# Performance work log

Measured on AMD Instinct MI355X. Metric: run time of the kernel, lower is better.

## Reference

```python
import jax, jax.numpy as jnp
import numpy as np

COUNT_BINS = 8
BOUND = 3.0
MIN_BIN_WIDTH = 1e-3
MIN_BIN_HEIGHT = 1e-3
MIN_DERIVATIVE = 1e-3
EPS = 1e-6


def _made_masks(D, H1, H2, M):
    indeg = np.arange(1, D + 1)                     # input degrees 1..D
    h1 = np.arange(H1) % (D - 1) + 1                # hidden degrees in [1, D-1]
    h2 = np.arange(H2) % (D - 1) + 1
    outdeg = np.tile(indeg, M)                      # (M*D,), reshape-compatible with (M, D)
    m1 = (h1[:, None] >= indeg[None, :]).astype(np.float32)   # (H1, D)
    m2 = (h2[:, None] >= h1[None, :]).astype(np.float32)      # (H2, H1)
    m3 = (outdeg[:, None] > h2[None, :]).astype(np.float32)   # (M*D, H2)
    return jnp.asarray(m1), jnp.asarray(m2), jnp.asarray(m3)


def _rq_spline_forward(x, w, h, d):
    # x: (B, D); w, h: (B, D, K) simplex weights; d: (B, D, K-1) softplus'd interior derivatives
    K = w.shape[-1]
    left, right = -BOUND, BOUND

    widths = MIN_BIN_WIDTH + (1.0 - MIN_BIN_WIDTH * K) * w
    heights = MIN_BIN_HEIGHT + (1.0 - MIN_BIN_HEIGHT * K) * h
    derivs = MIN_DERIVATIVE + d
    ones = jnp.ones_like(derivs[..., :1])
    derivs = jnp.concatenate([ones, derivs, ones], -1)          # (B, D, K+1), boundary slope 1

    cw = jnp.cumsum(widths, -1)
    edge_l = jnp.full_like(cw[..., :1], left)
    edge_r = jnp.full_like(cw[..., :1], right)
    cumw = jnp.concatenate([edge_l, left + (right - left) * cw[..., :-1], edge_r], -1)  # (B, D, K+1)
    widths = cumw[..., 1:] - cumw[..., :-1]
    ch = jnp.cumsum(heights, -1)
    cumh = jnp.concatenate([edge_l, left + (right - left) * ch[..., :-1], edge_r], -1)
    heights = cumh[..., 1:] - cumh[..., :-1]

    inside = (x >= left) & (x <= right)
    xc = jnp.clip(x, left, right)
    # pyro: bin_idx = sum(x >= cumwidths + eps) - 1
    idx = jnp.sum((xc[..., None] >= (cumw + EPS)).astype(jnp.int32), -1) - 1
    idx = jnp.clip(idx, 0, K - 1)                               # (B, D)

    def g(t):
        return jnp.take_along_axis(t, idx[..., None], axis=-1)[..., 0]

    x_k, w_k = g(cumw), g(widths)
    y_k, h_k = g(cumh), g(heights)
    delta = h_k / w_k
    d_k, d_k1 = g(derivs), g(derivs[..., 1:])

    theta = (xc - x_k) / w_k
    tt = theta * (1.0 - theta)
    num = h_k * (delta * theta ** 2 + d_k * tt)
    den = delta + (d_k + d_k1 - 2.0 * delta) * tt
    y = y_k + num / den
    dnum = delta ** 2 * (d_k1 * theta ** 2 + 2.0 * delta * tt + d_k * (1.0 - theta) ** 2)
    ld = jnp.log(dnum) - 2.0 * jnp.log(den)
    return jnp.where(inside, y, x), jnp.where(inside, ld, jnp.zeros_like(ld))


def _forward(x, W1, b1, W2, b2, W3, b3):
    B, D = x.shape
    H1, H2 = W1.shape[0], W2.shape[0]
    K = COUNT_BINS
    M = 3 * K - 1
    m1, m2, m3 = _made_masks(D, H1, H2, M)
    h1 = jax.nn.relu(x @ (W1 * m1).T + b1)
    h2 = jax.nn.relu(h1 @ (W2 * m2).T + b2)
    p = (h2 @ (W3 * m3).T + b3).reshape(B, M, D)                # (B, 3K-1, D)
    w = jax.nn.softmax(jnp.swapaxes(p[:, :K, :], 1, 2), axis=-1)          # (B, D, K)
    hgt = jax.nn.softmax(jnp.swapaxes(p[:, K:2 * K, :], 1, 2), axis=-1)   # (B, D, K)
    d = jax.nn.softplus(jnp.swapaxes(p[:, 2 * K:, :], 1, 2))              # (B, D, K-1)
    z, ld = _rq_spline_forward(x, w, hgt, d)
    return z, ld.sum(-1)


def setup_inputs() -> dict:
    key = jax.random.key(0)
    ks = jax.random.split(key, 7)
    B, D, H1, H2 = 32768, 64, 64, 32
    M = 3 * COUNT_BINS - 1
    s1, s2, s3 = 1.0 / np.sqrt(D), 1.0 / np.sqrt(H1), 1.0 / np.sqrt(H2)
    return {
        "x": jax.random.normal(ks[0], (B, D), jnp.float32),
        "W1": jax.random.uniform(ks[1], (H1, D), jnp.float32, -s1, s1),
        "b1": jax.random.uniform(ks[2], (H1,), jnp.float32, -s1, s1),
        "W2": jax.random.uniform(ks[3], (H2, H1), jnp.float32, -s2, s2),
        "b2": jax.random.uniform(ks[4], (H2,), jnp.float32, -s2, s2),
        "W3": jax.random.uniform(ks[5], (M * D, H2), jnp.float32, -s3, s3),
        "b3": jax.random.uniform(ks[6], (M * D,), jnp.float32, -s3, s3),
    }


def reference(x, W1, b1, W2, b2, W3, b3):
    return _forward(x, W1, b1, W2, b2, W3, b3)
```

## Files before the change

### kernel.cpp

```cpp
#include <hip/hip_runtime.h>

#define NM 23

typedef short short8 __attribute__((ext_vector_type(8)));
typedef float f32x4 __attribute__((ext_vector_type(4)));

__device__ __forceinline__ float softplus_f(float v) {
  return fmaxf(v, 0.f) + __logf(1.f + __expf(-fabsf(v)));
}

__device__ __forceinline__ float fastrcp(float v) {
  return __builtin_amdgcn_rcpf(v);
}

__device__ __forceinline__ unsigned short bf16_rne(float x) {
  unsigned u = __float_as_uint(x);
  u += 0x7FFFu + ((u >> 16) & 1u);
  return (unsigned short)(u >> 16);
}

__global__ __launch_bounds__(256) void prep_kernel(
    const float* __restrict__ W1, const float* __restrict__ W2,
    const float* __restrict__ W3,
    unsigned short* __restrict__ B1hi, unsigned short* __restrict__ B1lo,
    unsigned short* __restrict__ B2hi, unsigned short* __restrict__ B2lo,
    unsigned short* __restrict__ B3hi, unsigned short* __restrict__ B3lo) {
  const int idx = blockIdx.x * 256 + threadIdx.x;
  const int j = idx & 7, lane = (idx >> 3) & 63;
  const int col = lane & 15, quad = lane >> 4;

  if (idx < 4096) {
    const int rest = idx >> 9, kt = rest & 1, nt = rest >> 1;
    const int k = kt * 32 + quad * 8 + j;
    const int n = nt * 16 + col;
    const float v = ((n % 63) >= k) ? W1[n * 64 + k] : 0.f;
    const unsigned short h = bf16_rne(v);
    B1hi[idx] = h;
    B1lo[idx] = bf16_rne(v - __uint_as_float(((unsigned)h) << 16));
  }
  if (idx < 2048) {
    const int rest = idx >> 9, kt = rest & 1, nt = rest >> 1;
    const int k = kt * 32 + quad * 8 + j;
    const int n = nt * 16 + col;
    const float v = ((k % 63) <= n) ? W2[n * 64 + k] : 0.f;
    const unsigned short h = bf16_rne(v);
    B2hi[idx] = h;
    B2lo[idx] = bf16_rne(v - __uint_as_float(((unsigned)h) << 16));
  }
  if (idx < 92 * 64 * 8) {
    const int nt = idx >> 9;
    const int n = nt * 16 + col;
    const int d = n & 63;
    const int k = quad * 8 + j;
    const float v = (k < d) ? W3[(size_t)n * 32 + k] : 0.f;
    const unsigned short h = bf16_rne(v);
    B3hi[idx] = h;
    B3lo[idx] = bf16_rne(v - __uint_as_float(((unsigned)h) << 16));
  }
}

__device__ __forceinline__ void cvt_hilo(const float* src, short8& hi,
                                         short8& lo) {
  const f32x4 a0 = *reinterpret_cast<const f32x4*>(src);
  const f32x4 a1 = *reinterpret_cast<const f32x4*>(src + 4);
  const float af[8] = {a0.x, a0.y, a0.z, a0.w, a1.x, a1.y, a1.z, a1.w};
  #pragma unroll
  for (int j = 0; j < 8; ++j) {
    const unsigned short h = bf16_rne(af[j]);
    hi[j] = (short)h;
    lo[j] = (short)bf16_rne(af[j] - __uint_as_float(((unsigned)h) << 16));
  }
}

__global__ __launch_bounds__(256, 4) void fused_kernel(
    const float* __restrict__ x,
    const unsigned short* __restrict__ B1hi,
    const unsigned short* __restrict__ B1lo,
    const float* __restrict__ b1,
    const unsigned short* __restrict__ B2hi,
    const unsigned short* __restrict__ B2lo,
    const float* __restrict__ b2,
    const unsigned short* __restrict__ B3hi,
    const unsigned short* __restrict__ B3lo,
    const float* __restrict__ b3,
    float* __restrict__ out, int B) {
  __shared__ float h1s[64][68];
  __shared__ float h2s[64][36];
  __shared__ float b3s[64 * NM];

  const int t = threadIdx.x;
  const int b0 = blockIdx.x * 64;

  for (int idx = t; idx < 64 * NM; idx += 256) {
    const int dl = idx / NM, m = idx - dl * NM;
    b3s[idx] = b3[m * 64 + dl];
  }
  __syncthreads();

  const int lane = t & 63;
  const int wv   = __builtin_amdgcn_readfirstlane(t >> 6);
  const int mt   = wv;
  const int col  = lane & 15;
  const int quad = lane >> 4;
  const int arow = mt * 16 + col;

  {
    const float* xrow = x + (size_t)(b0 + arow) * 64;
    short8 ahi[2], alo[2];
    #pragma unroll
    for (int kt = 0; kt < 2; ++kt)
      cvt_hilo(xrow + kt * 32 + quad * 8, ahi[kt], alo[kt]);

    #pragma unroll
    for (int nt = 0; nt < 4; ++nt) {
      const float bv = b1[nt * 16 + col];
      f32x4 acc = {bv, bv, bv, bv};
      #pragma unroll
      for (int kt = 0; kt < 2; ++kt) {
        const size_t off = ((size_t)(nt * 2 + kt) * 64 + lane) * 8;
        const short8 bh = *reinterpret_cast<const short8*>(B1hi + off);
        const short8 bl = *reinterpret_cast<const short8*>(B1lo + off);
        acc = __builtin_amdgcn_mfma_f32_16x16x32_bf16(ahi[kt], bh, acc, 0, 0, 0);
        acc = __builtin_amdgcn_mfma_f32_16x16x32_bf16(alo[kt], bh, acc, 0, 0, 0);
        acc = __builtin_amdgcn_mfma_f32_16x16x32_bf16(ahi[kt], bl, acc, 0, 0, 0);
      }
      #pragma unroll
      for (int reg = 0; reg < 4; ++reg)
        h1s[mt * 16 + quad * 4 + reg][nt * 16 + col] = fmaxf(acc[reg], 0.f);
    }
  }

  {
    short8 ahi[2], alo[2];
    #pragma unroll
    for (int kt = 0; kt < 2; ++kt)
      cvt_hilo(&h1s[arow][kt * 32 + quad * 8], ahi[kt], alo[kt]);

    #pragma unroll
    for (int nt = 0; nt < 2; ++nt) {
      const float bv = b2[nt * 16 + col];
      f32x4 acc = {bv, bv, bv, bv};
      #pragma unroll
      for (int kt = 0; kt < 2; ++kt) {
        const size_t off = ((size_t)(nt * 2 + kt) * 64 + lane) * 8;
        const short8 bh = *reinterpret_cast<const short8*>(B2hi + off);
        const short8 bl = *reinterpret_cast<const short8*>(B2lo + off);
        acc = __builtin_amdgcn_mfma_f32_16x16x32_bf16(ahi[kt], bh, acc, 0, 0, 0);
        acc = __builtin_amdgcn_mfma_f32_16x16x32_bf16(alo[kt], bh, acc, 0, 0, 0);
        acc = __builtin_amdgcn_mfma_f32_16x16x32_bf16(ahi[kt], bl, acc, 0, 0, 0);
      }
      #pragma unroll
      for (int reg = 0; reg < 4; ++reg)
        h2s[mt * 16 + quad * 4 + reg][nt * 16 + col] = fmaxf(acc[reg], 0.f);
    }
  }

  short8 ahi, alo;
  cvt_hilo(&h2s[arow][quad * 8], ahi, alo);

  float ldr[4] = {0.f, 0.f, 0.f, 0.f};
  const float* xg = x + (size_t)b0 * 64;
  float* zg = out + (size_t)b0 * 64;
  const int row0 = mt * 16 + quad * 4;
  const float WSC = 1.0f - 1e-3f * 8.0f;

  #pragma unroll 1
  for (int dc = 0; dc < 4; ++dc) {
    const int d = dc * 16 + col;

    float xvv[4];
    #pragma unroll
    for (int reg = 0; reg < 4; ++reg)
      xvv[reg] = xg[(size_t)(row0 + reg) * 64 + d];

    float xcv[4], fidx[4], xkv[4], wkv[4], ykv[4], hkv[4];

    {
      f32x4 acc[8];
      #pragma unroll
      for (int m = 0; m < 8; ++m) {
        const float bv = b3s[d * NM + m];
        acc[m] = (f32x4){bv, bv, bv, bv};
      }
      #pragma unroll
      for (int m = 0; m < 8; ++m) {
        const size_t off = ((size_t)(4 * m + dc) * 64 + lane) * 8;
        const short8 bh = *reinterpret_cast<const short8*>(B3hi + off);
        const short8 bl = *reinterpret_cast<const short8*>(B3lo + off);
        acc[m] = __builtin_amdgcn_mfma_f32_16x16x32_bf16(ahi, bh, acc[m], 0, 0, 0);
        acc[m] = __builtin_amdgcn_mfma_f32_16x16x32_bf16(alo, bh, acc[m], 0, 0, 0);
        acc[m] = __builtin_amdgcn_mfma_f32_16x16x32_bf16(ahi, bl, acc[m], 0, 0, 0);
      }
      #pragma unroll
      for (int reg = 0; reg < 4; ++reg) {
        float ew[8], sw = 0.f;
        #pragma unroll
        for (int k = 0; k < 8; ++k) { ew[k] = __expf(acc[k][reg]); sw += ew[k]; }
        const float invw = fastrcp(sw);
        float cumw[9];
        cumw[0] = -3.f;
        float cw = 0.f;
        #pragma unroll
        for (int k = 0; k < 7; ++k) {
          cw += 1e-3f + WSC * (ew[k] * invw);
          cumw[k + 1] = fmaf(6.f, cw, -3.f);
        }
        cumw[8] = 3.f;

        const float xv = xvv[reg];
        const float xc = fminf(fmaxf(xv, -3.f), 3.f);
        float fi = 0.f, xk = cumw[0], xk1 = cumw[1];
        #pragma unroll
        for (int k = 1; k < 8; ++k) {
          const bool s = xc >= cumw[k] + 1e-6f;
          xk  = s ? cumw[k]     : xk;
          xk1 = s ? cumw[k + 1] : xk1;
          fi  = s ? (float)k    : fi;
        }
        xcv[reg] = xc; fidx[reg] = fi; xkv[reg] = xk; wkv[reg] = xk1 - xk;
      }
    }

    {
      f32x4 acc[8];
      #pragma unroll
      for (int m = 0; m < 8; ++m) {
        const float bv = b3s[d * NM + (8 + m)];
        acc[m] = (f32x4){bv, bv, bv, bv};
      }
      #pragma unroll
      for (int m = 0; m < 8; ++m) {
        const size_t off = ((size_t)(4 * (8 + m) + dc) * 64 + lane) * 8;
        const short8 bh = *reinterpret_cast<const short8*>(B3hi + off);
        const short8 bl = *reinterpret_cast<const short8*>(B3lo + off);
        acc[m] = __builtin_amdgcn_mfma_f32_16x16x32_bf16(ahi, bh, acc[m], 0, 0, 0);
        acc[m] = __builtin_amdgcn_mfma_f32_16x16x32_bf16(alo, bh, acc[m], 0, 0, 0);
        acc[m] = __builtin_amdgcn_mfma_f32_16x16x32_bf16(ahi, bl, acc[m], 0, 0, 0);
      }
      #pragma unroll
      for (int reg = 0; reg < 4; ++reg) {
        float eh[8], sh = 0.f;
        #pragma unroll
        for (int k = 0; k < 8; ++k) { eh[k] = __expf(acc[k][reg]); sh += eh[k]; }
        const float invh = fastrcp(sh);
        float cumh[9];
        cumh[0] = -3.f;
        float ch = 0.f;
        #pragma unroll
        for (int k = 0; k < 7; ++k) {
          ch += 1e-3f + WSC * (eh[k] * invh);
          cumh[k + 1] = fmaf(6.f, ch, -3.f);
        }
        cumh[8] = 3.f;

        float yk = cumh[0], yk1 = cumh[1];
        #pragma unroll
        for (int k = 1; k < 8; ++k) {
          const bool s = fidx[reg] >= (float)k;
          yk  = s ? cumh[k]     : yk;
          yk1 = s ? cumh[k + 1] : yk1;
        }
        ykv[reg] = yk; hkv[reg] = yk1 - yk;
      }
    }

    {
      f32x4 acc[7];
      #pragma unroll
      for (int m = 0; m < 7; ++m) {
        const float bv = b3s[d * NM + (16 + m)];
        acc[m] = (f32x4){bv, bv, bv, bv};
      }
      #pragma unroll
      for (int m = 0; m < 7; ++m) {
        const size_t off = ((size_t)(4 * (16 + m) + dc) * 64 + lane) * 8;
        const short8 bh = *reinterpret_cast<const short8*>(B3hi + off);
        const short8 bl = *reinterpret_cast<const short8*>(B3lo + off);
        acc[m] = __builtin_amdgcn_mfma_f32_16x16x32_bf16(ahi, bh, acc[m], 0, 0, 0);
        acc[m] = __builtin_amdgcn_mfma_f32_16x16x32_bf16(alo, bh, acc[m], 0, 0, 0);
        acc[m] = __builtin_amdgcn_mfma_f32_16x16x32_bf16(ahi, bl, acc[m], 0, 0, 0);
      }
      #pragma unroll
      for (int reg = 0; reg < 4; ++reg) {
        float p[7];
        #pragma unroll
        for (int k = 0; k < 7; ++k) p[k] = acc[k][reg];
        const float fi = fidx[reg];

        float pa = p[0], pb = p[0];
        #pragma unroll
        for (int k = 2; k < 8; ++k) pa = (fi >= (float)k) ? p[k - 1] : pa;
        #pragma unroll
        for (int k = 1; k < 7; ++k) pb = (fi >= (float)k) ? p[k] : pb;
        const float spa = 1e-3f + softplus_f(pa);
        const float spb = 1e-3f + softplus_f(pb);
        const float dk  = (fi >= 0.5f) ? spa : 1.f;
        const float dk1 = (fi >= 6.5f) ? 1.f : spb;

        const float xc = xcv[reg], xk = xkv[reg], wk = wkv[reg];
        const float yk = ykv[reg], hk = hkv[reg];
        const float invwk = fastrcp(wk);
        const float delta = hk * invwk;
        const float theta = (xc - xk) * invwk;
        const float omt = 1.f - theta;
        const float tt = theta * omt;
        const float th2 = theta * theta;
        const float num = hk * (delta * th2 + dk * tt);
        const float den = delta + (dk + dk1 - 2.f * delta) * tt;
        const float rden = fastrcp(den);
        const float yv = yk + num * rden;
        const float dnum =
            delta * delta * (dk1 * th2 + 2.f * delta * tt + dk * omt * omt);
        const float ldv = __logf(dnum * rden * rden);

        const float xv = xvv[reg];
        const bool inside = (xv >= -3.f) && (xv <= 3.f);
        zg[(size_t)(row0 + reg) * 64 + d] = inside ? yv : xv;
        ldr[reg] += inside ? ldv : 0.f;
      }
    }
  }

  #pragma unroll
  for (int mask = 1; mask <= 8; mask <<= 1) {
    #pragma unroll
    for (int reg = 0; reg < 4; ++reg)
      ldr[reg] += __shfl_xor(ldr[reg], mask, 64);
  }

  if (col == 0) {
    #pragma unroll
    for (int reg = 0; reg < 4; ++reg)
      out[(size_t)B * 64 + b0 + row0 + reg] = ldr[reg];
  }
}

extern "C" void kernel_launch(void* const* d_in, const int* in_sizes, int n_in,
                              void* d_out, int out_size, void* d_ws, size_t ws_size,
                              hipStream_t stream) {
  const float* x  = (const float*)d_in[0];
  const float* W1 = (const float*)d_in[1];
  const float* b1 = (const float*)d_in[2];
  const float* W2 = (const float*)d_in[3];
  const float* b2 = (const float*)d_in[4];
  const float* W3 = (const float*)d_in[5];
  const float* b3 = (const float*)d_in[6];
  float* out = (float*)d_out;
  char* ws   = (char*)d_ws;

  unsigned short* B1hi = (unsigned short*)(ws);
  unsigned short* B1lo = (unsigned short*)(ws + 8192);
  unsigned short* B2hi = (unsigned short*)(ws + 16384);
  unsigned short* B2lo = (unsigned short*)(ws + 20480);
  unsigned short* B3hi = (unsigned short*)(ws + 24576);
  unsigned short* B3lo = (unsigned short*)(ws + 118784);

  const int B = in_sizes[0] / 64;

  prep_kernel<<<184, 256, 0, stream>>>(W1, W2, W3, B1hi, B1lo, B2hi, B2lo,
                                       B3hi, B3lo);

  fused_kernel<<<B / 64, 256, 0, stream>>>(
      x, B1hi, B1lo, b1, B2hi, B2lo, b2, B3hi, B3lo, b3, out, B);
}
```

Baseline: 118.2 us.

## Stage x tile and z output through shared memory with coalesced float4 accesses

```diff
diff --git a/kernel.cpp b/kernel.cpp
--- a/kernel.cpp
+++ b/kernel.cpp
@@ -84,13 +84,22 @@
     const unsigned short* __restrict__ B3lo,
     const float* __restrict__ b3,
     float* __restrict__ out, int B) {
-  __shared__ float h1s[64][68];
+  __shared__ float xs[64][68];
   __shared__ float h2s[64][36];
   __shared__ float b3s[64 * NM];
 
   const int t = threadIdx.x;
   const int b0 = blockIdx.x * 64;
 
+  #pragma unroll
+  for (int u = 0; u < 4; ++u) {
+    const int idx = t + u * 256;
+    const int rr = idx >> 4, c4 = (idx & 15) * 4;
+    const float4 v = *reinterpret_cast<const float4*>(
+        x + (size_t)b0 * 64 + (size_t)idx * 4);
+    xs[rr][c4 + 0] = v.x; xs[rr][c4 + 1] = v.y;
+    xs[rr][c4 + 2] = v.z; xs[rr][c4 + 3] = v.w;
+  }
   for (int idx = t; idx < 64 * NM; idx += 256) {
     const int dl = idx / NM, m = idx - dl * NM;
     b3s[idx] = b3[m * 64 + dl];
@@ -103,13 +112,20 @@
   const int col  = lane & 15;
   const int quad = lane >> 4;
   const int arow = mt * 16 + col;
+  const int row0 = mt * 16 + quad * 4;
+
+  float xvv[4][4];
+  #pragma unroll
+  for (int dc = 0; dc < 4; ++dc)
+    #pragma unroll
+    for (int reg = 0; reg < 4; ++reg)
+      xvv[dc][reg] = xs[row0 + reg][dc * 16 + col];
 
   {
-    const float* xrow = x + (size_t)(b0 + arow) * 64;
     short8 ahi[2], alo[2];
     #pragma unroll
     for (int kt = 0; kt < 2; ++kt)
-      cvt_hilo(xrow + kt * 32 + quad * 8, ahi[kt], alo[kt]);
+      cvt_hilo(&xs[arow][kt * 32 + quad * 8], ahi[kt], alo[kt]);
 
     #pragma unroll
     for (int nt = 0; nt < 4; ++nt) {
@@ -126,7 +142,7 @@
       }
       #pragma unroll
       for (int reg = 0; reg < 4; ++reg)
-        h1s[mt * 16 + quad * 4 + reg][nt * 16 + col] = fmaxf(acc[reg], 0.f);
+        xs[row0 + reg][nt * 16 + col] = fmaxf(acc[reg], 0.f);
     }
   }
 
@@ -134,7 +150,7 @@
     short8 ahi[2], alo[2];
     #pragma unroll
     for (int kt = 0; kt < 2; ++kt)
-      cvt_hilo(&h1s[arow][kt * 32 + quad * 8], ahi[kt], alo[kt]);
+      cvt_hilo(&xs[arow][kt * 32 + quad * 8], ahi[kt], alo[kt]);
 
     #pragma unroll
     for (int nt = 0; nt < 2; ++nt) {
@@ -151,7 +167,7 @@
       }
       #pragma unroll
       for (int reg = 0; reg < 4; ++reg)
-        h2s[mt * 16 + quad * 4 + reg][nt * 16 + col] = fmaxf(acc[reg], 0.f);
+        h2s[row0 + reg][nt * 16 + col] = fmaxf(acc[reg], 0.f);
     }
   }
 
@@ -159,19 +175,11 @@
   cvt_hilo(&h2s[arow][quad * 8], ahi, alo);
 
   float ldr[4] = {0.f, 0.f, 0.f, 0.f};
-  const float* xg = x + (size_t)b0 * 64;
-  float* zg = out + (size_t)b0 * 64;
-  const int row0 = mt * 16 + quad * 4;
   const float WSC = 1.0f - 1e-3f * 8.0f;
 
   #pragma unroll 1
   for (int dc = 0; dc < 4; ++dc) {
     const int d = dc * 16 + col;
-
-    float xvv[4];
-    #pragma unroll
-    for (int reg = 0; reg < 4; ++reg)
-      xvv[reg] = xg[(size_t)(row0 + reg) * 64 + d];
 
     float xcv[4], fidx[4], xkv[4], wkv[4], ykv[4], hkv[4];
 
@@ -207,7 +215,7 @@
         }
         cumw[8] = 3.f;
 
-        const float xv = xvv[reg];
+        const float xv = xvv[dc][reg];
         const float xc = fminf(fmaxf(xv, -3.f), 3.f);
         float fi = 0.f, xk = cumw[0], xk1 = cumw[1];
         #pragma unroll
@@ -313,9 +321,9 @@
             delta * delta * (dk1 * th2 + 2.f * delta * tt + dk * omt * omt);
         const float ldv = __logf(dnum * rden * rden);
 
-        const float xv = xvv[reg];
+        const float xv = xvv[dc][reg];
         const bool inside = (xv >= -3.f) && (xv <= 3.f);
-        zg[(size_t)(row0 + reg) * 64 + d] = inside ? yv : xv;
+        xs[row0 + reg][d] = inside ? yv : xv;
         ldr[reg] += inside ? ldv : 0.f;
       }
     }
@@ -332,6 +340,17 @@
     #pragma unroll
     for (int reg = 0; reg < 4; ++reg)
       out[(size_t)B * 64 + b0 + row0 + reg] = ldr[reg];
+  }
+
+  __syncthreads();
+
+  #pragma unroll
+  for (int u = 0; u < 4; ++u) {
+    const int idx = t + u * 256;
+    const int rr = idx >> 4, c4 = (idx & 15) * 4;
+    const float4 v = make_float4(xs[rr][c4 + 0], xs[rr][c4 + 1],
+                                 xs[rr][c4 + 2], xs[rr][c4 + 3]);
+    *reinterpret_cast<float4*>(out + (size_t)(b0 + rr) * 64 + c4) = v;
   }
 }
 
```

Result: no change. 117.5 us (-0.6%).

## Split work across 8 waves per 32-row block and stage output via LDS

Applied to the files above, without the earlier changes.

```diff
diff --git a/kernel.cpp b/kernel.cpp
--- a/kernel.cpp
+++ b/kernel.cpp
@@ -4,6 +4,8 @@
 
 typedef short short8 __attribute__((ext_vector_type(8)));
 typedef float f32x4 __attribute__((ext_vector_type(4)));
+
+#define LOG2E 1.44269504088896340736f
 
 __device__ __forceinline__ float softplus_f(float v) {
   return fmaxf(v, 0.f) + __logf(1.f + __expf(-fabsf(v)));
@@ -51,8 +53,10 @@
     const int nt = idx >> 9;
     const int n = nt * 16 + col;
     const int d = n & 63;
+    const int m = n >> 6;
     const int k = quad * 8 + j;
-    const float v = (k < d) ? W3[(size_t)n * 32 + k] : 0.f;
+    float v = (k < d) ? W3[(size_t)n * 32 + k] : 0.f;
+    if (m < 16) v *= LOG2E;
     const unsigned short h = bf16_rne(v);
     B3hi[idx] = h;
     B3lo[idx] = bf16_rne(v - __uint_as_float(((unsigned)h) << 16));
@@ -72,7 +76,7 @@
   }
 }
 
-__global__ __launch_bounds__(256, 4) void fused_kernel(
+__global__ __launch_bounds__(512, 4) void fused_kernel(
     const float* __restrict__ x,
     const unsigned short* __restrict__ B1hi,
     const unsigned short* __restrict__ B1lo,
@@ -84,240 +88,236 @@
     const unsigned short* __restrict__ B3lo,
     const float* __restrict__ b3,
     float* __restrict__ out, int B) {
-  __shared__ float h1s[64][68];
-  __shared__ float h2s[64][36];
+  __shared__ float h1s[32][68];
+  __shared__ float h2s[32][68];
   __shared__ float b3s[64 * NM];
+  __shared__ float ldp[4][32];
 
   const int t = threadIdx.x;
-  const int b0 = blockIdx.x * 64;
-
-  for (int idx = t; idx < 64 * NM; idx += 256) {
+  const int b0 = blockIdx.x * 32;
+
+  for (int idx = t; idx < 64 * NM; idx += 512) {
     const int dl = idx / NM, m = idx - dl * NM;
-    b3s[idx] = b3[m * 64 + dl];
+    const float s = (m < 16) ? LOG2E : 1.f;
+    b3s[idx] = b3[m * 64 + dl] * s;
   }
   __syncthreads();
 
   const int lane = t & 63;
   const int wv   = __builtin_amdgcn_readfirstlane(t >> 6);
-  const int mt   = wv;
   const int col  = lane & 15;
   const int quad = lane >> 4;
-  const int arow = mt * 16 + col;
-
-  {
-    const float* xrow = x + (size_t)(b0 + arow) * 64;
+
+  {
+    const int mt1 = wv >> 2, nt1 = wv & 3;
+    const float* xrow = x + (size_t)(b0 + mt1 * 16 + col) * 64;
     short8 ahi[2], alo[2];
     #pragma unroll
     for (int kt = 0; kt < 2; ++kt)
       cvt_hilo(xrow + kt * 32 + quad * 8, ahi[kt], alo[kt]);
 
-    #pragma unroll
-    for (int nt = 0; nt < 4; ++nt) {
-      const float bv = b1[nt * 16 + col];
-      f32x4 acc = {bv, bv, bv, bv};
-      #pragma unroll
-      for (int kt = 0; kt < 2; ++kt) {
-        const size_t off = ((size_t)(nt * 2 + kt) * 64 + lane) * 8;
-        const short8 bh = *reinterpret_cast<const short8*>(B1hi + off);
-        const short8 bl = *reinterpret_cast<const short8*>(B1lo + off);
-        acc = __builtin_amdgcn_mfma_f32_16x16x32_bf16(ahi[kt], bh, acc, 0, 0, 0);
-        acc = __builtin_amdgcn_mfma_f32_16x16x32_bf16(alo[kt], bh, acc, 0, 0, 0);
-        acc = __builtin_amdgcn_mfma_f32_16x16x32_bf16(ahi[kt], bl, acc, 0, 0, 0);
+    const float bv = b1[nt1 * 16 + col];
+    f32x4 acc = {bv, bv, bv, bv};
+    #pragma unroll
+    for (int kt = 0; kt < 2; ++kt) {
+      const size_t off = ((size_t)(nt1 * 2 + kt) * 64 + lane) * 8;
+      const short8 bh = *reinterpret_cast<const short8*>(B1hi + off);
+      const short8 bl = *reinterpret_cast<const short8*>(B1lo + off);
+      acc = __builtin_amdgcn_mfma_f32_16x16x32_bf16(ahi[kt], bh, acc, 0, 0, 0);
+      acc = __builtin_amdgcn_mfma_f32_16x16x32_bf16(alo[kt], bh, acc, 0, 0, 0);
+      acc = __builtin_amdgcn_mfma_f32_16x16x32_bf16(ahi[kt], bl, acc, 0, 0, 0);
+    }
+    #pragma unroll
+    for (int reg = 0; reg < 4; ++reg)
+      h1s[mt1 * 16 + quad * 4 + reg][nt1 * 16 + col] = fmaxf(acc[reg], 0.f);
+  }
+  __syncthreads();
+
+  if (wv < 4) {
+    const int mt2 = wv >> 1, nt2 = wv & 1;
+    short8 ahi[2], alo[2];
+    #pragma unroll
+    for (int kt = 0; kt < 2; ++kt)
+      cvt_hilo(&h1s[mt2 * 16 + col][kt * 32 + quad * 8], ahi[kt], alo[kt]);
+
+    const float bv = b2[nt2 * 16 + col];
+    f32x4 acc = {bv, bv, bv, bv};
+    #pragma unroll
+    for (int kt = 0; kt < 2; ++kt) {
+      const size_t off = ((size_t)(nt2 * 2 + kt) * 64 + lane) * 8;
+      const short8 bh = *reinterpret_cast<const short8*>(B2hi + off);
+      const short8 bl = *reinterpret_cast<const short8*>(B2lo + off);
+      acc = __builtin_amdgcn_mfma_f32_16x16x32_bf16(ahi[kt], bh, acc, 0, 0, 0);
+      acc = __builtin_amdgcn_mfma_f32_16x16x32_bf16(alo[kt], bh, acc, 0, 0, 0);
+      acc = __builtin_amdgcn_mfma_f32_16x16x32_bf16(ahi[kt], bl, acc, 0, 0, 0);
+    }
+    #pragma unroll
+    for (int reg = 0; reg < 4; ++reg)
+      h2s[mt2 * 16 + quad * 4 + reg][nt2 * 16 + col] = fmaxf(acc[reg], 0.f);
+  }
+  __syncthreads();
+
+  const int mt = wv >> 2, dc = wv & 3;
+  const int row0 = mt * 16 + quad * 4;
+  const int d = dc * 16 + col;
+
+  short8 ahi, alo;
+  cvt_hilo(&h2s[mt * 16 + col][quad * 8], ahi, alo);
+
+  float xvv[4];
+  #pragma unroll
+  for (int reg = 0; reg < 4; ++reg)
+    xvv[reg] = x[(size_t)(b0 + row0 + reg) * 64 + d];
+
+  __syncthreads();
+
+  float ldr[4] = {0.f, 0.f, 0.f, 0.f};
+  const float WSC = 1.0f - 1e-3f * 8.0f;
+
+  float xcv[4], fidx[4], xkv[4], wkv[4], ykv[4], hkv[4];
+
+  {
+    f32x4 acc[8];
+    #pragma unroll
+    for (int m = 0; m < 8; ++m) {
+      const float bv = b3s[d * NM + m];
+      acc[m] = (f32x4){bv, bv, bv, bv};
+    }
+    #pragma unroll
+    for (int m = 0; m < 8; ++m) {
+      const size_t off = ((size_t)(4 * m + dc) * 64 + lane) * 8;
+      const short8 bh = *reinterpret_cast<const short8*>(B3hi + off);
+      const short8 bl = *reinterpret_cast<const short8*>(B3lo + off);
+      acc[m] = __builtin_amdgcn_mfma_f32_16x16x32_bf16(ahi, bh, acc[m], 0, 0, 0);
+      acc[m] = __builtin_amdgcn_mfma_f32_16x16x32_bf16(alo, bh, acc[m], 0, 0, 0);
+      acc[m] = __builtin_amdgcn_mfma_f32_16x16x32_bf16(ahi, bl, acc[m], 0, 0, 0);
+    }
+    #pragma unroll
+    for (int reg = 0; reg < 4; ++reg) {
+      float ew[8], sw = 0.f;
+      #pragma unroll
+      for (int k = 0; k < 8; ++k) { ew[k] = exp2f(acc[k][reg]); sw += ew[k]; }
+      const float invw = fastrcp(sw);
+      float cumw[9];
+      cumw[0] = -3.f;
+      float cw = 0.f;
+      #pragma unroll
+      for (int k = 0; k < 7; ++k) {
+        cw += 1e-3f + WSC * (ew[k] * invw);
+        cumw[k + 1] = fmaf(6.f, cw, -3.f);
       }
-      #pragma unroll
-      for (int reg = 0; reg < 4; ++reg)
-        h1s[mt * 16 + quad * 4 + reg][nt * 16 + col] = fmaxf(acc[reg], 0.f);
-    }
-  }
-
-  {
-    short8 ahi[2], alo[2];
-    #pragma unroll
-    for (int kt = 0; kt < 2; ++kt)
-      cvt_hilo(&h1s[arow][kt * 32 + quad * 8], ahi[kt], alo[kt]);
-
-    #pragma unroll
-    for (int nt = 0; nt < 2; ++nt) {
-      const float bv = b2[nt * 16 + col];
-      f32x4 acc = {bv, bv, bv, bv};
-      #pragma unroll
-      for (int kt = 0; kt < 2; ++kt) {
-        const size_t off = ((size_t)(nt * 2 + kt) * 64 + lane) * 8;
-        const short8 bh = *reinterpret_cast<const short8*>(B2hi + off);
-        const short8 bl = *reinterpret_cast<const short8*>(B2lo + off);
-        acc = __builtin_amdgcn_mfma_f32_16x16x32_bf16(ahi[kt], bh, acc, 0, 0, 0);
-        acc = __builtin_amdgcn_mfma_f32_16x16x32_bf16(alo[kt], bh, acc, 0, 0, 0);
-        acc = __builtin_amdgcn_mfma_f32_16x16x32_bf16(ahi[kt], bl, acc, 0, 0, 0);
+      cumw[8] = 3.f;
+
+      const float xv = xvv[reg];
+      const float xc = fminf(fmaxf(xv, -3.f), 3.f);
+      float fi = 0.f, xk = cumw[0], xk1 = cumw[1];
+      #pragma unroll
+      for (int k = 1; k < 8; ++k) {
+        const bool s = xc >= cumw[k] + 1e-6f;
+        xk  = s ? cumw[k]     : xk;
+        xk1 = s ? cumw[k + 1] : xk1;
+        fi  = s ? (float)k    : fi;
       }
-      #pragma unroll
-      for (int reg = 0; reg < 4; ++reg)
-        h2s[mt * 16 + quad * 4 + reg][nt * 16 + col] = fmaxf(acc[reg], 0.f);
-    }
-  }
-
-  short8 ahi, alo;
-  cvt_hilo(&h2s[arow][quad * 8], ahi, alo);
-
-  float ldr[4] = {0.f, 0.f, 0.f, 0.f};
-  const float* xg = x + (size_t)b0 * 64;
-  float* zg = out + (size_t)b0 * 64;
-  const int row0 = mt * 16 + quad * 4;
-  const float WSC = 1.0f - 1e-3f * 8.0f;
-
-  #pragma unroll 1
-  for (int dc = 0; dc < 4; ++dc) {
-    const int d = dc * 16 + col;
-
-    float xvv[4];
-    #pragma unroll
-    for (int reg = 0; reg < 4; ++reg)
-      xvv[reg] = xg[(size_t)(row0 + reg) * 64 + d];
-
-    float xcv[4], fidx[4], xkv[4], wkv[4], ykv[4], hkv[4];
-
-    {
-      f32x4 acc[8];
-      #pragma unroll
-      for (int m = 0; m < 8; ++m) {
-        const float bv = b3s[d * NM + m];
-        acc[m] = (f32x4){bv, bv, bv, bv};
+      xcv[reg] = xc; fidx[reg] = fi; xkv[reg] = xk; wkv[reg] = xk1 - xk;
+    }
+  }
+
+  {
+    f32x4 acc[8];
+    #pragma unroll
+    for (int m = 0; m < 8; ++m) {
+      const float bv = b3s[d * NM + (8 + m)];
+      acc[m] = (f32x4){bv, bv, bv, bv};
+    }
+    #pragma unroll
+    for (int m = 0; m < 8; ++m) {
+      const size_t off = ((size_t)(4 * (8 + m) + dc) * 64 + lane) * 8;
+      const short8 bh = *reinterpret_cast<const short8*>(B3hi + off);
+      const short8 bl = *reinterpret_cast<const short8*>(B3lo + off);
+      acc[m] = __builtin_amdgcn_mfma_f32_16x16x32_bf16(ahi, bh, acc[m], 0, 0, 0);
+      acc[m] = __builtin_amdgcn_mfma_f32_16x16x32_bf16(alo, bh, acc[m], 0, 0, 0);
+      acc[m] = __builtin_amdgcn_mfma_f32_16x16x32_bf16(ahi, bl, acc[m], 0, 0, 0);
+    }
+    #pragma unroll
+    for (int reg = 0; reg < 4; ++reg) {
+      float eh[8], sh = 0.f;
+      #pragma unroll
+      for (int k = 0; k < 8; ++k) { eh[k] = exp2f(acc[k][reg]); sh += eh[k]; }
+      const float invh = fastrcp(sh);
+      float cumh[9];
+      cumh[0] = -3.f;
+      float ch = 0.f;
+      #pragma unroll
+      for (int k = 0; k < 7; ++k) {
+        ch += 1e-3f + WSC * (eh[k] * invh);
+        cumh[k + 1] = fmaf(6.f, ch, -3.f);
       }
-      #pragma unroll
-      for (int m = 0; m < 8; ++m) {
-        const size_t off = ((size_t)(4 * m + dc) * 64 + lane) * 8;
-        const short8 bh = *reinterpret_cast<const short8*>(B3hi + off);
-        const short8 bl = *reinterpret_cast<const short8*>(B3lo + off);
-        acc[m] = __builtin_amdgcn_mfma_f32_16x16x32_bf16(ahi, bh, acc[m], 0, 0, 0);
-        acc[m] = __builtin_amdgcn_mfma_f32_16x16x32_bf16(alo, bh, acc[m], 0, 0, 0);
-        acc[m] = __builtin_amdgcn_mfma_f32_16x16x32_bf16(ahi, bl, acc[m], 0, 0, 0);
+      cumh[8] = 3.f;
+
+      float yk = cumh[0], yk1 = cumh[1];
+      #pragma unroll
+      for (int k = 1; k < 8; ++k) {
+        const bool s = fidx[reg] >= (float)k;
+        yk  = s ? cumh[k]     : yk;
+        yk1 = s ? cumh[k + 1] : yk1;
       }
-      #pragma unroll
-      for (int reg = 0; reg < 4; ++reg) {
-        float ew[8], sw = 0.f;
-        #pragma unroll
-        for (int k = 0; k < 8; ++k) { ew[k] = __expf(acc[k][reg]); sw += ew[k]; }
-        const float invw = fastrcp(sw);
-        float cumw[9];
-        cumw[0] = -3.f;
-        float cw = 0.f;
-        #pragma unroll
-        for (int k = 0; k < 7; ++k) {
-          cw += 1e-3f + WSC * (ew[k] * invw);
-          cumw[k + 1] = fmaf(6.f, cw, -3.f);
-        }
-        cumw[8] = 3.f;
-
-        const float xv = xvv[reg];
-        const float xc = fminf(fmaxf(xv, -3.f), 3.f);
-        float fi = 0.f, xk = cumw[0], xk1 = cumw[1];
-        #pragma unroll
-        for (int k = 1; k < 8; ++k) {
-          const bool s = xc >= cumw[k] + 1e-6f;
-          xk  = s ? cumw[k]     : xk;
-          xk1 = s ? cumw[k + 1] : xk1;
-          fi  = s ? (float)k    : fi;
-        }
-        xcv[reg] = xc; fidx[reg] = fi; xkv[reg] = xk; wkv[reg] = xk1 - xk;
-      }
-    }
-
-    {
-      f32x4 acc[8];
-      #pragma unroll
-      for (int m = 0; m < 8; ++m) {
-        const float bv = b3s[d * NM + (8 + m)];
-        acc[m] = (f32x4){bv, bv, bv, bv};
-      }
-      #pragma unroll
-      for (int m = 0; m < 8; ++m) {
-        const size_t off = ((size_t)(4 * (8 + m) + dc) * 64 + lane) * 8;
-        const short8 bh = *reinterpret_cast<const short8*>(B3hi + off);
-        const short8 bl = *reinterpret_cast<const short8*>(B3lo + off);
-        acc[m] = __builtin_amdgcn_mfma_f32_16x16x32_bf16(ahi, bh, acc[m], 0, 0, 0);
-        acc[m] = __builtin_amdgcn_mfma_f32_16x16x32_bf16(alo, bh, acc[m], 0, 0, 0);
-        acc[m] = __builtin_amdgcn_mfma_f32_16x16x32_bf16(ahi, bl, acc[m], 0, 0, 0);
-      }
-      #pragma unroll
-      for (int reg = 0; reg < 4; ++reg) {
-        float eh[8], sh = 0.f;
-        #pragma unroll
-        for (int k = 0; k < 8; ++k) { eh[k] = __expf(acc[k][reg]); sh += eh[k]; }
-        const float invh = fastrcp(sh);
-        float cumh[9];
-        cumh[0] = -3.f;
-        float ch = 0.f;
-        #pragma unroll
-        for (int k = 0; k < 7; ++k) {
-          ch += 1e-3f + WSC * (eh[k] * invh);
-          cumh[k + 1] = fmaf(6.f, ch, -3.f);
-        }
-        cumh[8] = 3.f;
-
-        float yk = cumh[0], yk1 = cumh[1];
-        #pragma unroll
-        for (int k = 1; k < 8; ++k) {
-          const bool s = fidx[reg] >= (float)k;
-          yk  = s ? cumh[k]     : yk;
-          yk1 = s ? cumh[k + 1] : yk1;
-        }
-        ykv[reg] = yk; hkv[reg] = yk1 - yk;
-      }
-    }
-
-    {
-      f32x4 acc[7];
-      #pragma unroll
-      for (int m = 0; m < 7; ++m) {
-        const float bv = b3s[d * NM + (16 + m)];
-        acc[m] = (f32x4){bv, bv, bv, bv};
-      }
-      #pragma unroll
-      for (int m = 0; m < 7; ++m) {
-        const size_t off = ((size_t)(4 * (16 + m) + dc) * 64 + lane) * 8;
-        const short8 bh = *reinterpret_cast<const short8*>(B3hi + off);
-        const short8 bl = *reinterpret_cast<const short8*>(B3lo + off);
-        acc[m] = __builtin_amdgcn_mfma_f32_16x16x32_bf16(ahi, bh, acc[m], 0, 0, 0);
-        acc[m] = __builtin_amdgcn_mfma_f32_16x16x32_bf16(alo, bh, acc[m], 0, 0, 0);
-        acc[m] = __builtin_amdgcn_mfma_f32_16x16x32_bf16(ahi, bl, acc[m], 0, 0, 0);
-      }
-      #pragma unroll
-      for (int reg = 0; reg < 4; ++reg) {
-        float p[7];
-        #pragma unroll
-        for (int k = 0; k < 7; ++k) p[k] = acc[k][reg];
-        const float fi = fidx[reg];
-
-        float pa = p[0], pb = p[0];
-        #pragma unroll
-        for (int k = 2; k < 8; ++k) pa = (fi >= (float)k) ? p[k - 1] : pa;
-        #pragma unroll
-        for (int k = 1; k < 7; ++k) pb = (fi >= (float)k) ? p[k] : pb;
-        const float spa = 1e-3f + softplus_f(pa);
-        const float spb = 1e-3f + softplus_f(pb);
-        const float dk  = (fi >= 0.5f) ? spa : 1.f;
-        const float dk1 = (fi >= 6.5f) ? 1.f : spb;
-
-        const float xc = xcv[reg], xk = xkv[reg], wk = wkv[reg];
-        const float yk = ykv[reg], hk = hkv[reg];
-        const float invwk = fastrcp(wk);
-        const float delta = hk * invwk;
-        const float theta = (xc - xk) * invwk;
-        const float omt = 1.f - theta;
-        const float tt = theta * omt;
-        const float th2 = theta * theta;
-        const float num = hk * (delta * th2 + dk * tt);
-        const float den = delta + (dk + dk1 - 2.f * delta) * tt;
-        const float rden = fastrcp(den);
-        const float yv = yk + num * rden;
-        const float dnum =
-            delta * delta * (dk1 * th2 + 2.f * delta * tt + dk * omt * omt);
-        const float ldv = __logf(dnum * rden * rden);
-
-        const float xv = xvv[reg];
-        const bool inside = (xv >= -3.f) && (xv <= 3.f);
-        zg[(size_t)(row0 + reg) * 64 + d] = inside ? yv : xv;
-        ldr[reg] += inside ? ldv : 0.f;
-      }
+      ykv[reg] = yk; hkv[reg] = yk1 - yk;
+    }
+  }
+
+  {
+    f32x4 acc[7];
+    #pragma unroll
+    for (int m = 0; m < 7; ++m) {
+      const float bv = b3s[d * NM + (16 + m)];
+      acc[m] = (f32x4){bv, bv, bv, bv};
+    }
+    #pragma unroll
+    for (int m = 0; m < 7; ++m) {
+      const size_t off = ((size_t)(4 * (16 + m) + dc) * 64 + lane) * 8;
+      const short8 bh = *reinterpret_cast<const short8*>(B3hi + off);
+      const short8 bl = *reinterpret_cast<const short8*>(B3lo + off);
+      acc[m] = __builtin_amdgcn_mfma_f32_16x16x32_bf16(ahi, bh, acc[m], 0, 0, 0);
+      acc[m] = __builtin_amdgcn_mfma_f32_16x16x32_bf16(alo, bh, acc[m], 0, 0, 0);
+      acc[m] = __builtin_amdgcn_mfma_f32_16x16x32_bf16(ahi, bl, acc[m], 0, 0, 0);
+    }
+    #pragma unroll
+    for (int reg = 0; reg < 4; ++reg) {
+      float p[7];
+      #pragma unroll
+      for (int k = 0; k < 7; ++k) p[k] = acc[k][reg];
+      const float fi = fidx[reg];
+
+      float pa = p[0], pb = p[0];
+      #pragma unroll
+      for (int k = 2; k < 8; ++k) pa = (fi >= (float)k) ? p[k - 1] : pa;
+      #pragma unroll
+      for (int k = 1; k < 7; ++k) pb = (fi >= (float)k) ? p[k] : pb;
+      const float spa = 1e-3f + softplus_f(pa);
+      const float spb = 1e-3f + softplus_f(pb);
+      const float dk  = (fi >= 0.5f) ? spa : 1.f;
+      const float dk1 = (fi >= 6.5f) ? 1.f : spb;
+
+      const float xc = xcv[reg], xk = xkv[reg], wk = wkv[reg];
+      const float yk = ykv[reg], hk = hkv[reg];
+      const float invwk = fastrcp(wk);
+      const float delta = hk * invwk;
+      const float theta = (xc - xk) * invwk;
+      const float omt = 1.f - theta;
+      const float tt = theta * omt;
+      const float th2 = theta * theta;
+      const float num = hk * (delta * th2 + dk * tt);
+      const float den = delta + (dk + dk1 - 2.f * delta) * tt;
+      const float rden = fastrcp(den);
+      const float yv = yk + num * rden;
+      const float dnum =
+          delta * delta * (dk1 * th2 + 2.f * delta * tt + dk * omt * omt);
+      const float ldv = __logf(dnum * rden * rden);
+
+      const float xv = xvv[reg];
+      const bool inside = (xv >= -3.f) && (xv <= 3.f);
+      h2s[row0 + reg][d] = inside ? yv : xv;
+      ldr[reg] += inside ? ldv : 0.f;
     }
   }
 
@@ -327,11 +327,23 @@
     for (int reg = 0; reg < 4; ++reg)
       ldr[reg] += __shfl_xor(ldr[reg], mask, 64);
   }
-
   if (col == 0) {
     #pragma unroll
     for (int reg = 0; reg < 4; ++reg)
-      out[(size_t)B * 64 + b0 + row0 + reg] = ldr[reg];
+      ldp[dc][row0 + reg] = ldr[reg];
+  }
+
+  __syncthreads();
+
+  if (t < 32)
+    out[(size_t)B * 64 + b0 + t] =
+        (ldp[0][t] + ldp[1][t]) + (ldp[2][t] + ldp[3][t]);
+
+  {
+    const int rr = t >> 4, c4 = (t & 15) * 4;
+    const float4 v = make_float4(h2s[rr][c4 + 0], h2s[rr][c4 + 1],
+                                 h2s[rr][c4 + 2], h2s[rr][c4 + 3]);
+    *reinterpret_cast<float4*>(out + (size_t)(b0 + rr) * 64 + c4) = v;
   }
 }
 
@@ -360,6 +372,6 @@
   prep_kernel<<<184, 256, 0, stream>>>(W1, W2, W3, B1hi, B1lo, B2hi, B2lo,
                                        B3hi, B3lo);
 
-  fused_kernel<<<B / 64, 256, 0, stream>>>(
+  fused_kernel<<<B / 32, 512, 0, stream>>>(
       x, B1hi, B1lo, b1, B2hi, B2lo, b2, B3hi, B3lo, b3, out, B);
 }
```

Result: faster. 106.3 us (-10.0%).
